# Kernel optimization log

Hardware: AMD Instinct MI355X
Metric: run time of the kernel (lower is better)

## Reference

```python
import jax, jax.numpy as jnp
import numpy as np

DIM = 768
NUM_HEADS = 12
HEAD_DIM = DIM // NUM_HEADS
SCALE = HEAD_DIM ** -0.5


def setup_inputs() -> dict:
    key = jax.random.key(0)
    k_x, k_qkv, k_pw, k_pb = jax.random.split(key, 4)
    B, N = 2, 4096
    x = jax.random.normal(k_x, (B, N, DIM), dtype=jnp.float32)
    # Linear weights stored as [in, out] for x @ W
    w_qkv = jax.random.normal(k_qkv, (DIM, 3 * DIM), dtype=jnp.float32) * (DIM ** -0.5)
    w_proj = jax.random.normal(k_pw, (DIM, DIM), dtype=jnp.float32) * (DIM ** -0.5)
    b_proj = jax.random.normal(k_pb, (DIM,), dtype=jnp.float32) * 0.02
    return {"x": x, "w_qkv": w_qkv, "w_proj": w_proj, "b_proj": b_proj}


def reference(x, w_qkv, w_proj, b_proj):
    B, N, D = x.shape
    H, Hd = NUM_HEADS, HEAD_DIM
    qkv = (x @ w_qkv).reshape(B, N, 3, H, Hd)
    qkv = jnp.transpose(qkv, (2, 0, 3, 1, 4))  # [3, B, H, N, Hd]
    q, k, v = qkv[0], qkv[1], qkv[2]
    attn = jnp.einsum("bhnd,bhmd->bhnm", q, k) * SCALE  # [B,H,N,N]
    attn = jax.nn.softmax(attn, axis=-1)
    out = jnp.einsum("bhnm,bhmd->bhnd", attn, v)  # [B,H,N,Hd]
    out = jnp.transpose(out, (0, 2, 1, 3)).reshape(B, N, D)
    return out @ w_proj + b_proj
```

## Files before the change

### kernel.cpp

```cpp
#include <hip/hip_runtime.h>
#include <hip/hip_bf16.h>


#define NSEQ 4096
#define NTOK 8192
#define NHD  12
#define QSCALE 0.18033688011112043f

#define GSTR 36

typedef __attribute__((ext_vector_type(8))) __bf16 bf16x8;
typedef __attribute__((ext_vector_type(4))) __bf16 bf16x4;
typedef __attribute__((ext_vector_type(8))) unsigned short u16x8;
typedef __attribute__((ext_vector_type(4))) float  f32x4;

#if defined(__has_builtin)
#  if __has_builtin(__builtin_amdgcn_exp2f)
#    define EXP2(x) __builtin_amdgcn_exp2f(x)
#  else
#    define EXP2(x) exp2f(x)
#  endif
#else
#  define EXP2(x) exp2f(x)
#endif

__device__ inline f32x4 mfma16(bf16x8 a, bf16x8 b, f32x4 c) {
    return __builtin_amdgcn_mfma_f32_16x16x32_bf16(a, b, c, 0, 0, 0);
}

__global__ __launch_bounds__(256)
void wT_kernel(const float* __restrict__ W, __bf16* __restrict__ WT, int K, int N)
{
    __shared__ float t[32][33];
    const int tid = threadIdx.x;
    const int bk = blockIdx.x * 32, bn = blockIdx.y * 32;
    const int tx = tid & 31, ty = tid >> 5;
    #pragma unroll
    for (int i = 0; i < 4; ++i)
        t[ty + 8 * i][tx] = W[(size_t)(bk + ty + 8 * i) * N + bn + tx];
    __syncthreads();
    const int n = bn + (tid >> 3), kc = (tid & 7) * 4;
    bf16x4 w;
    #pragma unroll
    for (int j = 0; j < 4; ++j) w[j] = (__bf16)t[kc + j][tid >> 3];
    *(bf16x4*)(WT + (size_t)n * K + bk + kc) = w;
}

template<int A_BF16, int EPI>
__global__ __launch_bounds__(256)
void gemm_kernel(const void* __restrict__ Ap, const __bf16* __restrict__ BT,
                 const float* __restrict__ bias, void* __restrict__ Cp,
                 int M, int N, int K)
{
    __shared__ __bf16 lds_a [128 * GSTR];
    __shared__ __bf16 lds_bt[128 * GSTR];
    const int tid  = threadIdx.x;
    const int lane = tid & 63, wave = tid >> 6;
    const int l16  = lane & 15, lg = lane >> 4;
    const int wr = (wave >> 1) * 64, wc = (wave & 1) * 64;
    const int m0 = blockIdx.x * 128, n0 = blockIdx.y * 128;

    const int ar8 = tid >> 3, aq8 = tid & 7;
    const int r4  = tid >> 2, q4  = tid & 3;

    f32x4 areg[4]; bf16x8 aregb[2]; bf16x8 bregb[2];

    auto load_tiles = [&](int k0) {
        if constexpr (A_BF16) {
            const __bf16* A = (const __bf16*)Ap;
            #pragma unroll
            for (int i = 0; i < 2; ++i)
                aregb[i] = *(const bf16x8*)(A + (size_t)(m0 + r4 + i * 64) * K + k0 + q4 * 8);
        } else {
            const float* A = (const float*)Ap;
            #pragma unroll
            for (int i = 0; i < 4; ++i)
                areg[i] = *(const f32x4*)(A + (size_t)(m0 + ar8 + i * 32) * K + k0 + aq8 * 4);
        }
        #pragma unroll
        for (int i = 0; i < 2; ++i)
            bregb[i] = *(const bf16x8*)(BT + (size_t)(n0 + r4 + i * 64) * K + k0 + q4 * 8);
    };
    auto store_tiles = [&]() {
        if constexpr (A_BF16) {
            #pragma unroll
            for (int i = 0; i < 2; ++i)
                *(bf16x8*)&lds_a[(r4 + i * 64) * GSTR + q4 * 8] = aregb[i];
        } else {
            #pragma unroll
            for (int i = 0; i < 4; ++i) {
                bf16x4 w;
                #pragma unroll
                for (int c = 0; c < 4; ++c) w[c] = (__bf16)areg[i][c];
                *(bf16x4*)&lds_a[(ar8 + i * 32) * GSTR + aq8 * 4] = w;
            }
        }
        #pragma unroll
        for (int i = 0; i < 2; ++i)
            *(bf16x8*)&lds_bt[(r4 + i * 64) * GSTR + q4 * 8] = bregb[i];
    };

    f32x4 acc[4][4] = {};
    load_tiles(0);

    for (int k0 = 0; k0 < K; k0 += 32) {
        store_tiles();
        __syncthreads();
        if (k0 + 32 < K) load_tiles(k0 + 32);

        bf16x8 a[4], b[4];
        #pragma unroll
        for (int mf = 0; mf < 4; ++mf)
            a[mf] = *(const bf16x8*)&lds_a[(wr + mf * 16 + l16) * GSTR + lg * 8];
        #pragma unroll
        for (int nf = 0; nf < 4; ++nf)
            b[nf] = *(const bf16x8*)&lds_bt[(wc + nf * 16 + l16) * GSTR + lg * 8];
        __builtin_amdgcn_s_setprio(1);
        #pragma unroll
        for (int mf = 0; mf < 4; ++mf)
            #pragma unroll
            for (int nf = 0; nf < 4; ++nf)
                acc[mf][nf] = mfma16(a[mf], b[nf], acc[mf][nf]);
        __builtin_amdgcn_s_setprio(0);
        __syncthreads();
    }

    #pragma unroll
    for (int mf = 0; mf < 4; ++mf) {
        #pragma unroll
        for (int nf = 0; nf < 4; ++nf) {
            int n = n0 + wc + nf * 16 + l16;
            #pragma unroll
            for (int r = 0; r < 4; ++r) {
                int m = m0 + wr + mf * 16 + lg * 4 + r;
                float v = acc[mf][nf][r];
                if constexpr (EPI == 0) {
                    if (n < 768) v *= QSCALE;
                    ((__bf16*)Cp)[(size_t)m * N + n] = (__bf16)v;
                } else {
                    ((float*)Cp)[(size_t)m * N + n] = v + bias[n];
                }
            }
        }
    }
}

__global__ __launch_bounds__(256)
void attn_kernel(const __bf16* __restrict__ qkv, __bf16* __restrict__ out)
{
    __shared__ __bf16 k_lds[2][64 * 72];
    __shared__ __bf16 v_lds[2][64 * 64];
    __shared__ __bf16 p_lds[4][32 * 72];

    const int tid = threadIdx.x, lane = tid & 63, wave = tid >> 6;
    const int l16 = lane & 15, lg = lane >> 4;

    int bid = (blockIdx.x & 7) * 96 + (blockIdx.x >> 3);
    const int qt = bid & 31;
    const int h  = (bid >> 5) % NHD;
    const int b  = bid / (32 * NHD);
    const size_t rowbase = (size_t)b * NSEQ;
    const int q0 = qt * 128 + wave * 32;

    bf16x8 qf[2][2];
    #pragma unroll
    for (int mf = 0; mf < 2; ++mf)
        #pragma unroll
        for (int ks = 0; ks < 2; ++ks)
            qf[mf][ks] = *(const bf16x8*)(qkv + (rowbase + q0 + mf * 16 + l16) * 2304
                                              + h * 64 + ks * 32 + lg * 8);

    f32x4 o[4][2] = {};
    float l_r[2] = {0.f, 0.f};

    const int krow = tid >> 3, kq = tid & 7;
    const int vt   = tid >> 3, vq = tid & 7;
    u16x8 kreg0, kreg1, vreg0, vreg1;

    auto load_kv = [&](int kt) {
        const unsigned short* q16 = (const unsigned short*)qkv;
        size_t base = rowbase + (size_t)kt * 64;
        kreg0 = *(const u16x8*)(q16 + (base + krow)        * 2304 + 768  + h * 64 + kq * 8);
        kreg1 = *(const u16x8*)(q16 + (base + krow + 32)   * 2304 + 768  + h * 64 + kq * 8);
        vreg0 = *(const u16x8*)(q16 + (base + 2 * vt)      * 2304 + 1536 + h * 64 + vq * 8);
        vreg1 = *(const u16x8*)(q16 + (base + 2 * vt + 1)  * 2304 + 1536 + h * 64 + vq * 8);
    };
    auto store_kv = [&](int bsel) {
        *(u16x8*)&k_lds[bsel][krow * 72 + kq * 8]        = kreg0;
        *(u16x8*)&k_lds[bsel][(krow + 32) * 72 + kq * 8] = kreg1;
        #pragma unroll
        for (int j = 0; j < 8; ++j) {
            int d = vq * 8 + j;
            int chunk = ((vt >> 2) ^ d ^ (d >> 3)) & 7;
            unsigned int val = (unsigned int)vreg0[j] | ((unsigned int)vreg1[j] << 16);
            *(unsigned int*)((char*)&v_lds[bsel][0] + d * 128 + chunk * 16 + (vt & 3) * 4) = val;
        }
    };

    load_kv(0);
    store_kv(0);
    __syncthreads();

    const int NT = NSEQ / 64;
    for (int kt = 0; kt < NT; ++kt) {
        const int cur = kt & 1;
        if (kt + 1 < NT) load_kv(kt + 1);

        f32x4 sc[4][2] = {};
        __builtin_amdgcn_s_setprio(1);
        #pragma unroll
        for (int tf = 0; tf < 4; ++tf) {
            #pragma unroll
            for (int ks = 0; ks < 2; ++ks) {
                bf16x8 kfr = *(const bf16x8*)&k_lds[cur][(tf * 16 + l16) * 72 + ks * 32 + lg * 8];
                #pragma unroll
                for (int mf = 0; mf < 2; ++mf)
                    sc[tf][mf] = mfma16(kfr, qf[mf][ks], sc[tf][mf]);
            }
        }
        __builtin_amdgcn_s_setprio(0);

        #pragma unroll
        for (int mf = 0; mf < 2; ++mf) {
            float rs = 0.f;
            #pragma unroll
            for (int tf = 0; tf < 4; ++tf)
                #pragma unroll
                for (int r = 0; r < 4; ++r) {
                    float p = EXP2(sc[tf][mf][r]);
                    sc[tf][mf][r] = p;
                    rs += p;
                }
            l_r[mf] += rs;
        }

        __bf16* pl = p_lds[wave];
        #pragma unroll
        for (int mf = 0; mf < 2; ++mf)
            #pragma unroll
            for (int tf = 0; tf < 4; ++tf) {
                bf16x4 w;
                #pragma unroll
                for (int r = 0; r < 4; ++r) w[r] = (__bf16)sc[tf][mf][r];
                *(bf16x4*)&pl[(mf * 16 + l16) * 72 + tf * 16 + lg * 4] = w;
            }
        asm volatile("s_waitcnt lgkmcnt(0)" ::: "memory");

        __builtin_amdgcn_s_setprio(1);
        #pragma unroll
        for (int ks = 0; ks < 2; ++ks) {
            bf16x8 pf[2];
            #pragma unroll
            for (int mf = 0; mf < 2; ++mf)
                pf[mf] = *(const bf16x8*)&pl[(mf * 16 + l16) * 72 + ks * 32 + lg * 8];
            #pragma unroll
            for (int nf = 0; nf < 4; ++nf) {
                int d = nf * 16 + l16;
                int chunk = ((ks * 4 + lg) ^ d ^ (d >> 3)) & 7;
                bf16x8 vf = *(const bf16x8*)((const char*)&v_lds[cur][0] + d * 128 + chunk * 16);
                #pragma unroll
                for (int mf = 0; mf < 2; ++mf)
                    o[nf][mf] = mfma16(vf, pf[mf], o[nf][mf]);
            }
        }
        __builtin_amdgcn_s_setprio(0);

        if (kt + 1 < NT) store_kv(cur ^ 1);
        __syncthreads();
    }

    #pragma unroll
    for (int mf = 0; mf < 2; ++mf) {
        l_r[mf] += __shfl_xor(l_r[mf], 16);
        l_r[mf] += __shfl_xor(l_r[mf], 32);
        float inv = 1.0f / l_r[mf];
        size_t row = rowbase + q0 + mf * 16 + l16;
        #pragma unroll
        for (int nf = 0; nf < 4; ++nf) {
            bf16x4 w;
            #pragma unroll
            for (int r = 0; r < 4; ++r) w[r] = (__bf16)(o[nf][mf][r] * inv);
            *(bf16x4*)(out + row * 768 + h * 64 + nf * 16 + lg * 4) = w;
        }
    }
}

extern "C" void kernel_launch(void* const* d_in, const int* in_sizes, int n_in,
                              void* d_out, int out_size, void* d_ws, size_t ws_size,
                              hipStream_t stream)
{
    const float* x      = (const float*)d_in[0];
    const float* w_qkv  = (const float*)d_in[1];
    const float* w_proj = (const float*)d_in[2];
    const float* b_proj = (const float*)d_in[3];
    float* out = (float*)d_out;

    __bf16* qkv    = (__bf16*)d_ws;
    __bf16* attn   = qkv + (size_t)NTOK * 2304;
    __bf16* wqkvT  = attn;
    __bf16* wprojT = attn + (size_t)NTOK * 768;

    wT_kernel<<<dim3(24, 72), 256, 0, stream>>>(w_qkv, wqkvT, 768, 2304);
    wT_kernel<<<dim3(24, 24), 256, 0, stream>>>(w_proj, wprojT, 768, 768);

    gemm_kernel<0, 0><<<dim3(64, 18), 256, 0, stream>>>(x, wqkvT, nullptr, qkv,
                                                        NTOK, 3 * 768, 768);
    attn_kernel<<<dim3(2 * NHD * 32), 256, 0, stream>>>(qkv, attn);
    gemm_kernel<1, 1><<<dim3(64, 6), 256, 0, stream>>>(attn, wprojT, b_proj, out,
                                                       NTOK, 768, 768);
}
```

Before: 317.0 us.

## Load GEMM tiles straight into LDS and pre-convert x to bf16

The register-staged, software-prefetched GEMM tile loads are replaced with global_load_lds calls that write 16-byte chunks directly into unpadded shared-memory tiles. A separate kernel converts x to bf16 up front, using the output buffer as scratch, so both GEMMs read bf16 operands. The aim is to cut register traffic and VGPR pressure in the GEMM main loop. In exchange, the next-tile prefetch overlap and the LDS row padding are gone, so bank conflicts and exposed load latency may increase, and the extra conversion pass adds memory traffic.

```diff
diff --git a/kernel.cpp b/kernel.cpp
--- a/kernel.cpp
+++ b/kernel.cpp
@@ -7,12 +7,13 @@
 #define NHD  12
 #define QSCALE 0.18033688011112043f
 
-#define GSTR 36
-
 typedef __attribute__((ext_vector_type(8))) __bf16 bf16x8;
 typedef __attribute__((ext_vector_type(4))) __bf16 bf16x4;
 typedef __attribute__((ext_vector_type(8))) unsigned short u16x8;
 typedef __attribute__((ext_vector_type(4))) float  f32x4;
+
+typedef const __attribute__((address_space(1))) unsigned int* as1_u32p;
+typedef __attribute__((address_space(3))) unsigned int*       as3_u32p;
 
 #if defined(__has_builtin)
 #  if __has_builtin(__builtin_amdgcn_exp2f)
@@ -28,6 +29,22 @@
     return __builtin_amdgcn_mfma_f32_16x16x32_bf16(a, b, c, 0, 0, 0);
 }
 
+__device__ __forceinline__ void gload16(const __bf16* g, __bf16* l) {
+    __builtin_amdgcn_global_load_lds((as1_u32p)g, (as3_u32p)l, 16, 0, 0);
+}
+
+__global__ __launch_bounds__(256)
+void cvt_bf16_kernel(const float* __restrict__ x, __bf16* __restrict__ y)
+{
+    const size_t i = ((size_t)blockIdx.x * 256 + threadIdx.x) * 8;
+    f32x4 a = *(const f32x4*)(x + i);
+    f32x4 b = *(const f32x4*)(x + i + 4);
+    bf16x8 w;
+    #pragma unroll
+    for (int j = 0; j < 4; ++j) { w[j] = (__bf16)a[j]; w[4 + j] = (__bf16)b[j]; }
+    *(bf16x8*)(y + i) = w;
+}
+
 __global__ __launch_bounds__(256)
 void wT_kernel(const float* __restrict__ W, __bf16* __restrict__ WT, int K, int N)
 {
@@ -46,75 +63,41 @@
     *(bf16x4*)(WT + (size_t)n * K + bk + kc) = w;
 }
 
-template<int A_BF16, int EPI>
-__global__ __launch_bounds__(256)
-void gemm_kernel(const void* __restrict__ Ap, const __bf16* __restrict__ BT,
+template<int EPI>
+__global__ __launch_bounds__(256)
+void gemm_kernel(const __bf16* __restrict__ A, const __bf16* __restrict__ BT,
                  const float* __restrict__ bias, void* __restrict__ Cp,
                  int M, int N, int K)
 {
-    __shared__ __bf16 lds_a [128 * GSTR];
-    __shared__ __bf16 lds_bt[128 * GSTR];
+    __shared__ __bf16 lds_a[128 * 32];
+    __shared__ __bf16 lds_b[128 * 32];
     const int tid  = threadIdx.x;
     const int lane = tid & 63, wave = tid >> 6;
     const int l16  = lane & 15, lg = lane >> 4;
     const int wr = (wave >> 1) * 64, wc = (wave & 1) * 64;
     const int m0 = blockIdx.x * 128, n0 = blockIdx.y * 128;
 
-    const int ar8 = tid >> 3, aq8 = tid & 7;
-    const int r4  = tid >> 2, q4  = tid & 3;
-
-    f32x4 areg[4]; bf16x8 aregb[2]; bf16x8 bregb[2];
-
-    auto load_tiles = [&](int k0) {
-        if constexpr (A_BF16) {
-            const __bf16* A = (const __bf16*)Ap;
-            #pragma unroll
-            for (int i = 0; i < 2; ++i)
-                aregb[i] = *(const bf16x8*)(A + (size_t)(m0 + r4 + i * 64) * K + k0 + q4 * 8);
-        } else {
-            const float* A = (const float*)Ap;
-            #pragma unroll
-            for (int i = 0; i < 4; ++i)
-                areg[i] = *(const f32x4*)(A + (size_t)(m0 + ar8 + i * 32) * K + k0 + aq8 * 4);
-        }
-        #pragma unroll
-        for (int i = 0; i < 2; ++i)
-            bregb[i] = *(const bf16x8*)(BT + (size_t)(n0 + r4 + i * 64) * K + k0 + q4 * 8);
-    };
-    auto store_tiles = [&]() {
-        if constexpr (A_BF16) {
-            #pragma unroll
-            for (int i = 0; i < 2; ++i)
-                *(bf16x8*)&lds_a[(r4 + i * 64) * GSTR + q4 * 8] = aregb[i];
-        } else {
-            #pragma unroll
-            for (int i = 0; i < 4; ++i) {
-                bf16x4 w;
-                #pragma unroll
-                for (int c = 0; c < 4; ++c) w[c] = (__bf16)areg[i][c];
-                *(bf16x4*)&lds_a[(ar8 + i * 32) * GSTR + aq8 * 4] = w;
-            }
-        }
-        #pragma unroll
-        for (int i = 0; i < 2; ++i)
-            *(bf16x8*)&lds_bt[(r4 + i * 64) * GSTR + q4 * 8] = bregb[i];
-    };
-
     f32x4 acc[4][4] = {};
-    load_tiles(0);
 
     for (int k0 = 0; k0 < K; k0 += 32) {
-        store_tiles();
+        #pragma unroll
+        for (int i = 0; i < 2; ++i) {
+            const int s   = i * 256 + tid;
+            const int row = s >> 2, ch = s & 3;
+            __bf16* la = lds_a + (i * 256 + wave * 64) * 8;
+            __bf16* lb = lds_b + (i * 256 + wave * 64) * 8;
+            gload16(A  + (size_t)(m0 + row) * K + k0 + ch * 8, la);
+            gload16(BT + (size_t)(n0 + row) * K + k0 + ch * 8, lb);
+        }
         __syncthreads();
-        if (k0 + 32 < K) load_tiles(k0 + 32);
 
         bf16x8 a[4], b[4];
         #pragma unroll
         for (int mf = 0; mf < 4; ++mf)
-            a[mf] = *(const bf16x8*)&lds_a[(wr + mf * 16 + l16) * GSTR + lg * 8];
+            a[mf] = *(const bf16x8*)&lds_a[(wr + mf * 16 + l16) * 32 + lg * 8];
         #pragma unroll
         for (int nf = 0; nf < 4; ++nf)
-            b[nf] = *(const bf16x8*)&lds_bt[(wc + nf * 16 + l16) * GSTR + lg * 8];
+            b[nf] = *(const bf16x8*)&lds_b[(wc + nf * 16 + l16) * 32 + lg * 8];
         __builtin_amdgcn_s_setprio(1);
         #pragma unroll
         for (int mf = 0; mf < 4; ++mf)
@@ -244,7 +227,7 @@
                 for (int r = 0; r < 4; ++r) w[r] = (__bf16)sc[tf][mf][r];
                 *(bf16x4*)&pl[(mf * 16 + l16) * 72 + tf * 16 + lg * 4] = w;
             }
-        asm volatile("s_waitcnt lgkmcnt(0)" ::: "memory");
+    asm volatile("s_waitcnt lgkmcnt(0)" ::: "memory");
 
         __builtin_amdgcn_s_setprio(1);
         #pragma unroll
@@ -299,13 +282,15 @@
     __bf16* attn   = qkv + (size_t)NTOK * 2304;
     __bf16* wqkvT  = attn;
     __bf16* wprojT = attn + (size_t)NTOK * 768;
-
+    __bf16* x_bf16 = (__bf16*)d_out;
+
+    cvt_bf16_kernel<<<dim3(NTOK * 768 / (256 * 8)), 256, 0, stream>>>(x, x_bf16);
     wT_kernel<<<dim3(24, 72), 256, 0, stream>>>(w_qkv, wqkvT, 768, 2304);
     wT_kernel<<<dim3(24, 24), 256, 0, stream>>>(w_proj, wprojT, 768, 768);
 
-    gemm_kernel<0, 0><<<dim3(64, 18), 256, 0, stream>>>(x, wqkvT, nullptr, qkv,
-                                                        NTOK, 3 * 768, 768);
+    gemm_kernel<0><<<dim3(64, 18), 256, 0, stream>>>(x_bf16, wqkvT, nullptr, qkv,
+                                                     NTOK, 3 * 768, 768);
     attn_kernel<<<dim3(2 * NHD * 32), 256, 0, stream>>>(qkv, attn);
-    gemm_kernel<1, 1><<<dim3(64, 6), 256, 0, stream>>>(attn, wprojT, b_proj, out,
-                                                       NTOK, 768, 768);
-}
+    gemm_kernel<1><<<dim3(64, 6), 256, 0, stream>>>(attn, wprojT, b_proj, out,
+                                                    NTOK, 768, 768);
+}
```

New measurement: 316.5 us. No clear change (-0.2%).
